# Performance work log

Measured on AMD Instinct MI355X. Metric: run time of the kernel, lower is better.

## Reference

```python
import jax, jax.numpy as jnp
import numpy as np

B, P, ED, AD, DD, E, V, T = 64, 196, 2048, 512, 512, 300, 1000, 96


def setup_inputs() -> dict:
    key = jax.random.key(0)
    ks = jax.random.split(key, 24)
    s = 0.02  # small init scale for weights
    lens = jax.random.randint(ks[2], (B,), 2, T + 1).astype(jnp.int32)
    lens = lens.at[0].set(T)  # ensure max(decode_lengths) == T-1 (static)
    return {
        'encoder_out': jax.random.normal(ks[0], (B, P, ED), jnp.float32),
        'encoded_captions': jax.random.randint(ks[1], (B, T), 0, V),
        'caption_lengths': lens,
        'emb': jax.random.uniform(ks[3], (V, E), jnp.float32, -0.1, 0.1),
        'W_enc_att': jax.random.normal(ks[4], (ED, AD), jnp.float32) * s,
        'b_enc_att': jnp.zeros((AD,), jnp.float32),
        'W_dec_att': jax.random.normal(ks[5], (DD, AD), jnp.float32) * s,
        'b_dec_att': jnp.zeros((AD,), jnp.float32),
        'w_full': jax.random.normal(ks[6], (AD,), jnp.float32) * s,
        'b_full': jnp.zeros((), jnp.float32),
        'W_init_h': jax.random.normal(ks[7], (ED, DD), jnp.float32) * s,
        'b_init_h': jnp.zeros((DD,), jnp.float32),
        'W_init_c': jax.random.normal(ks[8], (ED, DD), jnp.float32) * s,
        'b_init_c': jnp.zeros((DD,), jnp.float32),
        'W_fbeta': jax.random.normal(ks[9], (DD, ED), jnp.float32) * s,
        'b_fbeta': jnp.zeros((ED,), jnp.float32),
        'W_ih': jax.random.normal(ks[10], (E + ED, 4 * DD), jnp.float32) * s,
        'b_ih': jnp.zeros((4 * DD,), jnp.float32),
        'W_hh': jax.random.normal(ks[11], (DD, 4 * DD), jnp.float32) * s,
        'b_hh': jnp.zeros((4 * DD,), jnp.float32),
        'W_fc': jax.random.uniform(ks[12], (DD, V), jnp.float32, -0.1, 0.1),
        'b_fc': jnp.zeros((V,), jnp.float32),
    }


def reference(encoder_out, encoded_captions, caption_lengths, emb,
              W_enc_att, b_enc_att, W_dec_att, b_dec_att, w_full, b_full,
              W_init_h, b_init_h, W_init_c, b_init_c, W_fbeta, b_fbeta,
              W_ih, b_ih, W_hh, b_hh, W_fc, b_fc):
    # Sort by caption length, descending (stable like torch.sort on ints)
    sort_ind = jnp.argsort(-caption_lengths)
    lens = caption_lengths[sort_ind]
    eo = encoder_out[sort_ind]                  # [B,P,ED]
    caps = encoded_captions[sort_ind]           # [B,T]
    decode_lengths = lens - 1                   # [B]

    embs = emb[caps]                            # [B,T,E]
    mean_eo = eo.mean(axis=1)                   # [B,ED]
    h0 = mean_eo @ W_init_h + b_init_h          # [B,DD]
    c0 = mean_eo @ W_init_c + b_init_c

    # encoder-side attention projection is step-invariant: hoist it
    att1 = eo @ W_enc_att + b_enc_att           # [B,P,AD]

    Tdec = T - 1
    ts = jnp.arange(Tdec)
    masks = (decode_lengths[None, :] > ts[:, None]).astype(eo.dtype)  # [Tdec,B]
    emb_seq = jnp.swapaxes(embs[:, :Tdec, :], 0, 1)                    # [Tdec,B,E]

    def step(carry, xs):
        h, c = carry
        emb_t, m = xs                           # [B,E], [B]
        mb = m[:, None]
        # Bahdanau attention
        att2 = h @ W_dec_att + b_dec_att        # [B,AD]
        e = jnp.einsum('bpa,a->bp', jax.nn.relu(att1 + att2[:, None, :]), w_full) + b_full
        alpha = jax.nn.softmax(e, axis=1)       # [B,P]
        awe = jnp.einsum('bpd,bp->bd', eo, alpha)  # [B,ED]
        gate = jax.nn.sigmoid(h @ W_fbeta + b_fbeta)
        x = jnp.concatenate([emb_t, gate * awe], axis=1)  # [B,E+ED]
        # LSTMCell (torch gate order: i, f, g, o)
        gates = x @ W_ih + b_ih + h @ W_hh + b_hh
        i, f, g, o = jnp.split(gates, 4, axis=1)
        c_new = jax.nn.sigmoid(f) * c + jax.nn.sigmoid(i) * jnp.tanh(g)
        h_new = jax.nn.sigmoid(o) * jnp.tanh(c_new)
        # only active rows (sorted so they are a prefix) update state
        h2 = mb * h_new + (1.0 - mb) * h
        c2 = mb * c_new + (1.0 - mb) * c
        preds = (h2 @ W_fc + b_fc) * mb         # dropout = identity (eval)
        return (h2, c2), (preds, alpha * mb)

    (_, _), (preds, alphas) = jax.lax.scan(step, (h0, c0), (emb_seq, masks))
    predictions = jnp.swapaxes(preds, 0, 1)     # [B,Tdec,V]
    alphas = jnp.swapaxes(alphas, 0, 1)         # [B,Tdec,P]
    return predictions, caps, decode_lengths, alphas, sort_ind
```

## Files before the change

kernel.cpp:

```cpp
#include <hip/hip_runtime.h>
#include <stddef.h>
#include <math.h>

static constexpr int B = 64, P = 196, ED = 2048, AD = 512, DD = 512, E = 300, V = 1000, T = 96, TD = 95;
static constexpr int KX = E + ED;
static constexpr int KTOT = KX + DD;
static constexpr int KSPLIT = 8;
static constexpr int KPER = 368;
static constexpr int NG = 4 * DD;
static constexpr int NC = 2560;

static constexpr size_t POFF   = 0;
static constexpr size_t CAPOFF = (size_t)B * TD * V;
static constexpr size_t DLOFF  = CAPOFF + (size_t)B * T;
static constexpr size_t AOFF   = DLOFF + B;
static constexpr size_t SOFF   = AOFF + (size_t)B * TD * P;

__device__ __forceinline__ float sigm(float x) { return 1.0f / (1.0f + expf(-x)); }

__global__ __launch_bounds__(64) void k_sort(const int* __restrict__ lens,
                                             const int* __restrict__ caps_in,
                                             int* __restrict__ sidx,
                                             int* __restrict__ dlen,
                                             int* __restrict__ caps_s,
                                             unsigned int* __restrict__ cnt,
                                             float* __restrict__ out) {
    __shared__ int sl[B];
    __shared__ int ss[B];
    int i = threadIdx.x;
    sl[i] = lens[i];
    cnt[i] = 0u;
    cnt[i + 64] = 0u;
    __syncthreads();
    int li = sl[i];
    int r = 0;
    for (int j = 0; j < B; j++) {
        int lj = sl[j];
        r += (lj > li) || (lj == li && j < i);
    }
    ss[r] = i;
    sidx[r] = i;
    dlen[r] = li - 1;
    out[DLOFF + r] = (float)(li - 1);
    out[SOFF + r] = (float)i;
    __syncthreads();
    for (int idx = i; idx < B * T; idx += B) {
        int b = idx / T, tt = idx % T;
        int v = caps_in[ss[b] * T + tt];
        caps_s[idx] = v;
        out[CAPOFF + idx] = (float)v;
    }
}

__global__ __launch_bounds__(256) void k_emball(const float* __restrict__ emb,
                                                const int* __restrict__ caps_s,
                                                float* __restrict__ embT) {
    int t = blockIdx.x;
    int k0 = blockIdx.y * 60;
    for (int l = threadIdx.x; l < 60 * 64; l += 256) {
        int r = l >> 6, b = l & 63;
        int k = k0 + r;
        int cap = caps_s[b * T + t];
        embT[((size_t)t * E + k) * B + b] = emb[(size_t)cap * E + k];
    }
}

__global__ __launch_bounds__(256) void k_mean(const float* __restrict__ eo,
                                              const int* __restrict__ sidx,
                                              float* __restrict__ mean_eo) {
    int b = blockIdx.y;
    int d = blockIdx.x * 256 + threadIdx.x;
    const float* base = eo + ((size_t)sidx[b] * P) * ED + d;
    float s = 0.f;
    for (int p = 0; p < P; p++) s += base[(size_t)p * ED];
    mean_eo[(size_t)b * ED + d] = s * (1.0f / (float)P);
}

__global__ __launch_bounds__(256) void k_init(const float* __restrict__ mean_eo,
                                              const float* __restrict__ Wh, const float* __restrict__ bh,
                                              const float* __restrict__ Wc, const float* __restrict__ bc,
                                              float* __restrict__ h0, float* __restrict__ c0,
                                              float* __restrict__ xT) {
    int idx = blockIdx.x * 256 + threadIdx.x;
    int b = idx >> 9, j = idx & 511;
    const float* m = mean_eo + (size_t)b * ED;
    float ah = bh[j], ac = bc[j];
    for (int k = 0; k < ED; k++) {
        float mv = m[k];
        ah += mv * Wh[(size_t)k * DD + j];
        ac += mv * Wc[(size_t)k * DD + j];
    }
    h0[idx] = ah;
    c0[idx] = ac;
    xT[(size_t)(KX + DD + j) * B + b] = ah;
}

__global__ __launch_bounds__(256) void k_att1(const float* __restrict__ eo,
                                              const float* __restrict__ W,
                                              const float* __restrict__ bias,
                                              const int* __restrict__ sidx,
                                              float* __restrict__ att1) {
    int m0 = blockIdx.x * 64, n0 = blockIdx.y * 64;
    __shared__ float sA[16][68];
    __shared__ float sB[16][68];
    int tid = threadIdx.x;
    int tx = tid & 15, ty = tid >> 4;
    float acc[4][4] = {};

    int la_m = tid >> 2;
    int la_k = (tid & 3) * 4;
    int lb_k = tid >> 4;
    int lb_n = (tid & 15) * 4;

    int mA = m0 + la_m;
    int bA = mA / P, pA = mA % P;
    const float* arow = eo + ((size_t)sidx[bA] * P + pA) * ED;

    for (int k0 = 0; k0 < ED; k0 += 16) {
        float4 av = *(const float4*)(arow + k0 + la_k);
        sA[la_k + 0][la_m] = av.x;
        sA[la_k + 1][la_m] = av.y;
        sA[la_k + 2][la_m] = av.z;
        sA[la_k + 3][la_m] = av.w;
        float4 bv = *(const float4*)(W + (size_t)(k0 + lb_k) * AD + n0 + lb_n);
        *(float4*)&sB[lb_k][lb_n] = bv;
        __syncthreads();
#pragma unroll
        for (int kk = 0; kk < 16; kk++) {
            float4 a4 = *(const float4*)&sA[kk][ty * 4];
            float4 b4 = *(const float4*)&sB[kk][tx * 4];
            float av_[4] = {a4.x, a4.y, a4.z, a4.w};
            float bv_[4] = {b4.x, b4.y, b4.z, b4.w};
#pragma unroll
            for (int i = 0; i < 4; i++)
#pragma unroll
                for (int j = 0; j < 4; j++) acc[i][j] += av_[i] * bv_[j];
        }
        __syncthreads();
    }
#pragma unroll
    for (int i = 0; i < 4; i++) {
        int m = m0 + ty * 4 + i;
        int n = n0 + tx * 4;
        float4 o;
        o.x = acc[i][0] + bias[n + 0];
        o.y = acc[i][1] + bias[n + 1];
        o.z = acc[i][2] + bias[n + 2];
        o.w = acc[i][3] + bias[n + 3];
        *(float4*)(att1 + (size_t)m * AD + n) = o;
    }
}

__global__ __launch_bounds__(256) void kA1(const float* __restrict__ hprev,
                                           const float* __restrict__ Wda,
                                           const float* __restrict__ Wfb,
                                           const float* __restrict__ bda,
                                           const float* __restrict__ bfb,
                                           float* __restrict__ part1,
                                           unsigned int* __restrict__ cnt1,
                                           float* __restrict__ att2g,
                                           float* __restrict__ fg) {
    int bx = blockIdx.x;
    int nb = bx >> 2, ks = bx & 3;
    int n0 = nb * 32;
    bool is_att = (n0 < AD);
    const float* W = is_att ? Wda : Wfb;
    int ld = is_att ? AD : ED;
    int colb = is_att ? n0 : n0 - AD;
    int kbase = ks * 128;
    int tid = threadIdx.x;
    __shared__ float sH[2][16][68];
    __shared__ float sW[2][16][36];
    __shared__ unsigned int sOld;
    float acc[4][2] = {};
    int tb = tid & 15, tn = tid >> 4;
    int hb = tid >> 2, hq = tid & 3;
    int wk = tid >> 3, wn = (tid & 7) * 4;

    float4 hreg = *(const float4*)(hprev + (size_t)hb * DD + kbase + hq * 4);
    float4 wreg = make_float4(0.f, 0.f, 0.f, 0.f);
    if (tid < 128) wreg = *(const float4*)(W + (size_t)(kbase + wk) * ld + colb + wn);
    sH[0][hq * 4 + 0][hb] = hreg.x;
    sH[0][hq * 4 + 1][hb] = hreg.y;
    sH[0][hq * 4 + 2][hb] = hreg.z;
    sH[0][hq * 4 + 3][hb] = hreg.w;
    if (tid < 128) *(float4*)&sW[0][wk][wn] = wreg;
    __syncthreads();

    for (int tl = 0; tl < 8; tl++) {
        int cur = tl & 1, nxt = cur ^ 1;
        if (tl < 7) {
            int k0 = kbase + (tl + 1) * 16;
            hreg = *(const float4*)(hprev + (size_t)hb * DD + k0 + hq * 4);
            if (tid < 128) wreg = *(const float4*)(W + (size_t)(k0 + wk) * ld + colb + wn);
        }
#pragma unroll
        for (int kk = 0; kk < 16; kk++) {
            float4 hv = *(const float4*)&sH[cur][kk][tb * 4];
            float w0 = sW[cur][kk][tn * 2 + 0];
            float w1 = sW[cur][kk][tn * 2 + 1];
            acc[0][0] += hv.x * w0; acc[0][1] += hv.x * w1;
            acc[1][0] += hv.y * w0; acc[1][1] += hv.y * w1;
            acc[2][0] += hv.z * w0; acc[2][1] += hv.z * w1;
            acc[3][0] += hv.w * w0; acc[3][1] += hv.w * w1;
        }
        if (tl < 7) {
            sH[nxt][hq * 4 + 0][hb] = hreg.x;
            sH[nxt][hq * 4 + 1][hb] = hreg.y;
            sH[nxt][hq * 4 + 2][hb] = hreg.z;
            sH[nxt][hq * 4 + 3][hb] = hreg.w;
            if (tid < 128) *(float4*)&sW[nxt][wk][wn] = wreg;
        }
        __syncthreads();
    }

#pragma unroll
    for (int i = 0; i < 4; i++)
#pragma unroll
        for (int j = 0; j < 2; j++) {
            int b = tb * 4 + i, n = n0 + tn * 2 + j;
            __hip_atomic_store(&part1[((size_t)ks * B + b) * NC + n], acc[i][j],
                               __ATOMIC_RELAXED, __HIP_MEMORY_SCOPE_AGENT);
        }
    __syncthreads();
    if (tid == 0)
        sOld = __hip_atomic_fetch_add(&cnt1[nb], 1u, __ATOMIC_ACQ_REL, __HIP_MEMORY_SCOPE_AGENT);
    __syncthreads();
    if (sOld != 3u) return;

    if (tid == 0)
        __hip_atomic_store(&cnt1[nb], 0u, __ATOMIC_RELAXED, __HIP_MEMORY_SCOPE_AGENT);
#pragma unroll
    for (int rep = 0; rep < 8; rep++) {
        int idx = rep * 256 + tid;
        int b = idx >> 5, nn = idx & 31;
        int n = n0 + nn;
        float s = 0.f;
#pragma unroll
        for (int k = 0; k < 4; k++)
            s += __hip_atomic_load(&part1[((size_t)k * B + b) * NC + n],
                                   __ATOMIC_RELAXED, __HIP_MEMORY_SCOPE_AGENT);
        if (is_att) att2g[(size_t)b * AD + n] = s + bda[n];
        else {
            int d = n - AD;
            fg[(size_t)b * ED + d] = sigm(s + bfb[d]);
        }
    }
}

__global__ __launch_bounds__(256) void kA2e(const float* __restrict__ att2g,
                                            const float* __restrict__ att1,
                                            const float* __restrict__ wf,
                                            const float* __restrict__ bfv,
                                            float* __restrict__ eW) {
    int bid = blockIdx.x;
    int b = bid >> 2, ch = bid & 3;
    int tid = threadIdx.x;
    __shared__ float sa2[AD];
    __shared__ float swf[AD];
    sa2[tid] = att2g[(size_t)b * AD + tid];
    sa2[tid + 256] = att2g[(size_t)b * AD + tid + 256];
    swf[tid] = wf[tid];
    swf[tid + 256] = wf[tid + 256];
    __syncthreads();

    int w = tid >> 6, lane = tid & 63;
    float bf0 = bfv[0];
    for (int pl = w; pl < 49; pl += 4) {
        int p = ch * 49 + pl;
        const float* row = att1 + ((size_t)b * P + p) * AD + lane * 8;
        float4 u0 = *(const float4*)row;
        float4 u1 = *(const float4*)(row + 4);
        float4 s0 = *(const float4*)&sa2[lane * 8];
        float4 s1 = *(const float4*)&sa2[lane * 8 + 4];
        float4 w0 = *(const float4*)&swf[lane * 8];
        float4 w1 = *(const float4*)&swf[lane * 8 + 4];
        float acc = fmaxf(u0.x + s0.x, 0.f) * w0.x + fmaxf(u0.y + s0.y, 0.f) * w0.y +
                    fmaxf(u0.z + s0.z, 0.f) * w0.z + fmaxf(u0.w + s0.w, 0.f) * w0.w +
                    fmaxf(u1.x + s1.x, 0.f) * w1.x + fmaxf(u1.y + s1.y, 0.f) * w1.y +
                    fmaxf(u1.z + s1.z, 0.f) * w1.z + fmaxf(u1.w + s1.w, 0.f) * w1.w;
#pragma unroll
        for (int mm = 32; mm >= 1; mm >>= 1) acc += __shfl_xor(acc, mm, 64);
        if (lane == 0) eW[(size_t)b * P + p] = acc + bf0;
    }
}

__global__ __launch_bounds__(256) void kB(const float* __restrict__ eo,
                                          const int* __restrict__ sidx,
                                          const float* __restrict__ eW,
                                          const float* __restrict__ fg,
                                          const int* __restrict__ dlen,
                                          float* __restrict__ xT,
                                          float* __restrict__ out, int t) {
    int b = blockIdx.y, ch = blockIdx.x, tid = threadIdx.x;
    __shared__ float se[256];
    __shared__ float red[256];
    __shared__ float sal[P];
    __shared__ float part[4][260];

    se[tid] = (tid < P) ? eW[(size_t)b * P + tid] : -1e30f;
    __syncthreads();
    red[tid] = se[tid];
    __syncthreads();
    for (int s = 128; s > 0; s >>= 1) {
        if (tid < s) red[tid] = fmaxf(red[tid], red[tid + s]);
        __syncthreads();
    }
    float mx = red[0];
    __syncthreads();
    float ex = (tid < P) ? expf(se[tid] - mx) : 0.f;
    red[tid] = ex;
    __syncthreads();
    for (int s = 128; s > 0; s >>= 1) {
        if (tid < s) red[tid] += red[tid + s];
        __syncthreads();
    }
    float inv = 1.0f / red[0];
    if (tid < P) {
        float a = ex * inv;
        sal[tid] = a;
        if (ch == 0) {
            float m = (dlen[b] > t) ? 1.f : 0.f;
            out[AOFF + ((size_t)b * TD + t) * P + tid] = a * m;
        }
    }
    __syncthreads();

    int pg = tid >> 6, lane = tid & 63;
    int d = ch * 256 + lane * 4;
    const float* base = eo + ((size_t)sidx[b] * P) * ED + d;
    float ax = 0.f, ay = 0.f, az = 0.f, aw = 0.f;
#pragma unroll 7
    for (int i = 0; i < 49; i++) {
        int p = pg + i * 4;
        float4 v = *(const float4*)(base + (size_t)p * ED);
        float a = sal[p];
        ax += v.x * a; ay += v.y * a; az += v.z * a; aw += v.w * a;
    }
    part[pg][lane * 4 + 0] = ax;
    part[pg][lane * 4 + 1] = ay;
    part[pg][lane * 4 + 2] = az;
    part[pg][lane * 4 + 3] = aw;
    __syncthreads();
    if (tid < 64) {
        int d0 = ch * 256 + tid * 4;
        float4 g = *(const float4*)(fg + (size_t)b * ED + d0);
        float s0 = part[0][tid * 4 + 0] + part[1][tid * 4 + 0] + part[2][tid * 4 + 0] + part[3][tid * 4 + 0];
        float s1 = part[0][tid * 4 + 1] + part[1][tid * 4 + 1] + part[2][tid * 4 + 1] + part[3][tid * 4 + 1];
        float s2 = part[0][tid * 4 + 2] + part[1][tid * 4 + 2] + part[2][tid * 4 + 2] + part[3][tid * 4 + 2];
        float s3 = part[0][tid * 4 + 3] + part[1][tid * 4 + 3] + part[2][tid * 4 + 3] + part[3][tid * 4 + 3];
        xT[(size_t)(E + d0 + 0) * B + b] = g.x * s0;
        xT[(size_t)(E + d0 + 1) * B + b] = g.y * s1;
        xT[(size_t)(E + d0 + 2) * B + b] = g.z * s2;
        xT[(size_t)(E + d0 + 3) * B + b] = g.w * s3;
    }
}

__global__ __launch_bounds__(256) void kCD(const float* __restrict__ xT,
                                           const float* __restrict__ embT_t,
                                           const float* __restrict__ xh_r,
                                           const float* __restrict__ Wih,
                                           const float* __restrict__ Whh,
                                           float* __restrict__ part,
                                           unsigned int* __restrict__ cntCD,
                                           const float* __restrict__ bih,
                                           const float* __restrict__ bhh,
                                           const float* __restrict__ h0,
                                           float* __restrict__ hseq,
                                           const float* __restrict__ cread,
                                           float* __restrict__ cwrite,
                                           const int* __restrict__ dlen,
                                           float* __restrict__ xh_w, int t) {
    int bx = blockIdx.x;
    int ks = bx >> 6, nb = bx & 63;
    int n0 = nb * 32;
    int tid = threadIdx.x;
    int tb = tid & 15, tn = tid >> 4;
    int wk = tid >> 3, wn = (tid & 7) * 4;
    __shared__ float sW[2][16][36];
    __shared__ unsigned int sOld;
    float acc[4][2] = {};
    int kbase = ks * KPER;

    auto ldw = [&](int tile) -> float4 {
        int kg = kbase + tile * 16 + wk;
        float4 wv = make_float4(0.f, 0.f, 0.f, 0.f);
        if (kg < KX) wv = *(const float4*)&Wih[(size_t)kg * NG + n0 + wn];
        else if (kg < KTOT) wv = *(const float4*)&Whh[(size_t)(kg - KX) * NG + n0 + wn];
        return wv;
    };

    float4 wreg = make_float4(0.f, 0.f, 0.f, 0.f);
    if (tid < 128) {
        wreg = ldw(0);
        *(float4*)&sW[0][wk][wn] = wreg;
    }
    __syncthreads();

    for (int tile = 0; tile < 23; tile++) {
        int cur = tile & 1, nxt = cur ^ 1;
        if (tile < 22 && tid < 128) wreg = ldw(tile + 1);
#pragma unroll
        for (int kk = 0; kk < 16; kk++) {
            int kg = kbase + tile * 16 + kk;
            float4 xv = make_float4(0.f, 0.f, 0.f, 0.f);
            if (kg < E) xv = *(const float4*)&embT_t[(size_t)kg * B + tb * 4];
            else if (kg < KX) xv = *(const float4*)&xT[(size_t)kg * B + tb * 4];
            else if (kg < KTOT) xv = *(const float4*)&xh_r[(size_t)(kg - KX) * B + tb * 4];
            float w0 = sW[cur][kk][tn * 2 + 0];
            float w1 = sW[cur][kk][tn * 2 + 1];
            acc[0][0] += xv.x * w0; acc[0][1] += xv.x * w1;
            acc[1][0] += xv.y * w0; acc[1][1] += xv.y * w1;
            acc[2][0] += xv.z * w0; acc[2][1] += xv.z * w1;
            acc[3][0] += xv.w * w0; acc[3][1] += xv.w * w1;
        }
        if (tile < 22 && tid < 128) *(float4*)&sW[nxt][wk][wn] = wreg;
        __syncthreads();
    }

#pragma unroll
    for (int i = 0; i < 4; i++)
#pragma unroll
        for (int j = 0; j < 2; j++) {
            int b = tb * 4 + i, lc = tn * 2 + j;
            __hip_atomic_store(&part[((size_t)ks * B + b) * NG + n0 + lc], acc[i][j],
                               __ATOMIC_RELAXED, __HIP_MEMORY_SCOPE_AGENT);
        }
    __syncthreads();
    int jg = nb & 15;
    if (tid == 0)
        sOld = __hip_atomic_fetch_add(&cntCD[jg], 1u, __ATOMIC_ACQ_REL, __HIP_MEMORY_SCOPE_AGENT);
    __syncthreads();
    if (sOld != 31u) return;

    if (tid == 0)
        __hip_atomic_store(&cntCD[jg], 0u, __ATOMIC_RELAXED, __HIP_MEMORY_SCOPE_AGENT);

    const float* holds = (t == 0) ? h0 : (hseq + (size_t)(t - 1) * B * DD);
#pragma unroll
    for (int rep = 0; rep < 8; rep++) {
        int idx = rep * 256 + tid;
        int bb = idx >> 5;
        int jj = idx & 31;
        int j = jg * 32 + jj;
        float g4[4];
#pragma unroll
        for (int g = 0; g < 4; g++) {
            float gv = bih[g * DD + j] + bhh[g * DD + j];
#pragma unroll
            for (int s = 0; s < KSPLIT; s++)
                gv += __hip_atomic_load(&part[((size_t)s * B + bb) * NG + g * 512 + j],
                                        __ATOMIC_RELAXED, __HIP_MEMORY_SCOPE_AGENT);
            g4[g] = gv;
        }
        float cold = cread[(size_t)bb * DD + j];
        float hold = holds[(size_t)bb * DD + j];
        float cnew = sigm(g4[1]) * cold + sigm(g4[0]) * tanhf(g4[2]);
        float hnew = sigm(g4[3]) * tanhf(cnew);
        bool m = dlen[bb] > t;
        float h2 = m ? hnew : hold;
        float c2 = m ? cnew : cold;
        hseq[(size_t)t * B * DD + (size_t)bb * DD + j] = h2;
        cwrite[(size_t)bb * DD + j] = c2;
        xh_w[(size_t)j * B + bb] = h2;
    }
}

__global__ __launch_bounds__(256) void k_predsall(const float* __restrict__ hseq,
                                                  const float* __restrict__ Wfc,
                                                  const float* __restrict__ bfc,
                                                  const int* __restrict__ dlen,
                                                  float* __restrict__ out) {
    int t = blockIdx.x;
    int n0 = blockIdx.y * 64;
    int tid = threadIdx.x;
    int tx = tid & 15, ty = tid >> 4;
    __shared__ float sA[16][68];
    __shared__ float sB[16][68];
    float acc[4][4] = {};
    const float* A = hseq + (size_t)t * B * DD;

    for (int k0 = 0; k0 < DD; k0 += 16) {
        {
            int b = tid >> 2, q = tid & 3;
            float4 hv = *(const float4*)(A + (size_t)b * DD + k0 + q * 4);
            sA[q * 4 + 0][b] = hv.x;
            sA[q * 4 + 1][b] = hv.y;
            sA[q * 4 + 2][b] = hv.z;
            sA[q * 4 + 3][b] = hv.w;
        }
        {
            int kk = tid >> 4, nn = (tid & 15) * 4;
            int c = n0 + nn;
            const float* wrow = Wfc + (size_t)(k0 + kk) * V;
            float4 wv;
            if (c + 3 < V) wv = *(const float4*)(wrow + c);
            else {
                wv.x = (c + 0 < V) ? wrow[c + 0] : 0.f;
                wv.y = (c + 1 < V) ? wrow[c + 1] : 0.f;
                wv.z = (c + 2 < V) ? wrow[c + 2] : 0.f;
                wv.w = (c + 3 < V) ? wrow[c + 3] : 0.f;
            }
            *(float4*)&sB[kk][nn] = wv;
        }
        __syncthreads();
#pragma unroll
        for (int kk = 0; kk < 16; kk++) {
            float4 a4 = *(const float4*)&sA[kk][ty * 4];
            float4 b4 = *(const float4*)&sB[kk][tx * 4];
            float av_[4] = {a4.x, a4.y, a4.z, a4.w};
            float bv_[4] = {b4.x, b4.y, b4.z, b4.w};
#pragma unroll
            for (int i = 0; i < 4; i++)
#pragma unroll
                for (int j = 0; j < 4; j++) acc[i][j] += av_[i] * bv_[j];
        }
        __syncthreads();
    }
#pragma unroll
    for (int i = 0; i < 4; i++) {
        int b = ty * 4 + i;
        bool m = dlen[b] > t;
#pragma unroll
        for (int j = 0; j < 4; j++) {
            int n = n0 + tx * 4 + j;
            if (n < V)
                out[POFF + ((size_t)b * TD + t) * V + n] = m ? (acc[i][j] + bfc[n]) : 0.f;
        }
    }
}

extern "C" void kernel_launch(void* const* d_in, const int* in_sizes, int n_in,
                              void* d_out, int out_size, void* d_ws, size_t ws_size,
                              hipStream_t stream) {
    const float* eo    = (const float*)d_in[0];
    const int*   caps  = (const int*)d_in[1];
    const int*   lens  = (const int*)d_in[2];
    const float* emb   = (const float*)d_in[3];
    const float* Wea   = (const float*)d_in[4];
    const float* bea   = (const float*)d_in[5];
    const float* Wda   = (const float*)d_in[6];
    const float* bda   = (const float*)d_in[7];
    const float* wfull = (const float*)d_in[8];
    const float* bfull = (const float*)d_in[9];
    const float* Wih_  = (const float*)d_in[10];
    const float* bih_  = (const float*)d_in[11];
    const float* Wic   = (const float*)d_in[12];
    const float* bic   = (const float*)d_in[13];
    const float* Wfb   = (const float*)d_in[14];
    const float* bfb   = (const float*)d_in[15];
    const float* Wih   = (const float*)d_in[16];
    const float* bih   = (const float*)d_in[17];
    const float* Whh   = (const float*)d_in[18];
    const float* bhh   = (const float*)d_in[19];
    const float* Wfc   = (const float*)d_in[20];
    const float* bfc   = (const float*)d_in[21];
    float* out = (float*)d_out;

    char* w = (char*)d_ws;
    auto carve = [&](size_t bytes) -> void* {
        void* p = (void*)w;
        w += (bytes + 255) & ~(size_t)255;
        return p;
    };
    int* sidx      = (int*)carve(B * 4);
    int* dlen      = (int*)carve(B * 4);
    int* caps_s    = (int*)carve((size_t)B * T * 4);
    unsigned int* cnt = (unsigned int*)carve(128 * 4);
    float* mean_eo = (float*)carve((size_t)B * ED * 4);
    float* h0      = (float*)carve((size_t)B * DD * 4);
    float* cb0     = (float*)carve((size_t)B * DD * 4);
    float* cb1     = (float*)carve((size_t)B * DD * 4);
    float* att1    = (float*)carve((size_t)B * P * AD * 4);
    float* eWb     = (float*)carve((size_t)B * P * 4);
    float* att2g   = (float*)carve((size_t)B * AD * 4);
    float* fg      = (float*)carve((size_t)B * ED * 4);
    float* xT      = (float*)carve((size_t)(KTOT + DD) * B * 4);
    float* part    = (float*)carve((size_t)KSPLIT * B * NG * 4);
    float* part1   = (float*)carve((size_t)4 * B * NC * 4);
    float* hseq    = (float*)carve((size_t)TD * B * DD * 4);
    float* embT    = (float*)carve((size_t)TD * E * B * 4);
    float* cb[2] = {cb0, cb1};
    unsigned int* cnt1  = cnt;
    unsigned int* cntCD = cnt + 96;

    k_sort<<<1, 64, 0, stream>>>(lens, caps, sidx, dlen, caps_s, cnt, out);
    k_emball<<<dim3(TD, 5), 256, 0, stream>>>(emb, caps_s, embT);
    k_mean<<<dim3(ED / 256, B), 256, 0, stream>>>(eo, sidx, mean_eo);
    k_init<<<(B * DD) / 256, 256, 0, stream>>>(mean_eo, Wih_, bih_, Wic, bic, h0, cb1, xT);
    k_att1<<<dim3((B * P) / 64, AD / 64), 256, 0, stream>>>(eo, Wea, bea, sidx, att1);

    for (int t = 0; t < TD; t++) {
        const float* hprev = (t == 0) ? h0 : (hseq + (size_t)(t - 1) * B * DD);
        kA1<<<320, 256, 0, stream>>>(hprev, Wda, Wfb, bda, bfb, part1, cnt1, att2g, fg);
        kA2e<<<256, 256, 0, stream>>>(att2g, att1, wfull, bfull, eWb);
        kB<<<dim3(8, B), 256, 0, stream>>>(eo, sidx, eWb, fg, dlen, xT, out, t);
        const float* xh_r = xT + (size_t)(KX + ((t + 1) & 1) * DD) * B;
        float*       xh_w = xT + (size_t)(KX + (t & 1) * DD) * B;
        kCD<<<512, 256, 0, stream>>>(xT, embT + (size_t)t * E * B, xh_r, Wih, Whh, part, cntCD,
                                     bih, bhh, h0, hseq, cb[(t + 1) & 1], cb[t & 1], dlen, xh_w, t);
    }
    k_predsall<<<dim3(TD, 16), 256, 0, stream>>>(hseq, Wfc, bfc, dlen, out);
}
```

Measured before the change: 16.87 ms.

## Fuse per-timestep kernels into one persistent cooperative kernel with grid syncs

Replaces the four kernel launches per decode step (95 steps, 380 launches) with one cooperative persistent kernel of 512 blocks. Each step runs the four phases separated by grid.sync(), and shared memory is reused through a union. The goal is to remove per-launch overhead and kernel-boundary drains in the sequential recurrence. In exchange, it depends on all 512 blocks being co-resident at launch_bounds(256,2) and adds grid-wide barrier cost. Phases with fewer active blocks leave the other blocks idle.

```diff
diff --git a/kernel.cpp b/kernel.cpp
--- a/kernel.cpp
+++ b/kernel.cpp
@@ -1,6 +1,9 @@
 #include <hip/hip_runtime.h>
+#include <hip/hip_cooperative_groups.h>
 #include <stddef.h>
 #include <math.h>
+
+namespace cg = cooperative_groups;
 
 static constexpr int B = 64, P = 196, ED = 2048, AD = 512, DD = 512, E = 300, V = 1000, T = 96, TD = 95;
 static constexpr int KX = E + ED;
@@ -151,318 +154,312 @@
     }
 }
 
-__global__ __launch_bounds__(256) void kA1(const float* __restrict__ hprev,
-                                           const float* __restrict__ Wda,
-                                           const float* __restrict__ Wfb,
-                                           const float* __restrict__ bda,
-                                           const float* __restrict__ bfb,
-                                           float* __restrict__ part1,
-                                           unsigned int* __restrict__ cnt1,
-                                           float* __restrict__ att2g,
-                                           float* __restrict__ fg) {
-    int bx = blockIdx.x;
-    int nb = bx >> 2, ks = bx & 3;
-    int n0 = nb * 32;
-    bool is_att = (n0 < AD);
-    const float* W = is_att ? Wda : Wfb;
-    int ld = is_att ? AD : ED;
-    int colb = is_att ? n0 : n0 - AD;
-    int kbase = ks * 128;
-    int tid = threadIdx.x;
-    __shared__ float sH[2][16][68];
-    __shared__ float sW[2][16][36];
-    __shared__ unsigned int sOld;
-    float acc[4][2] = {};
-    int tb = tid & 15, tn = tid >> 4;
-    int hb = tid >> 2, hq = tid & 3;
-    int wk = tid >> 3, wn = (tid & 7) * 4;
-
-    float4 hreg = *(const float4*)(hprev + (size_t)hb * DD + kbase + hq * 4);
-    float4 wreg = make_float4(0.f, 0.f, 0.f, 0.f);
-    if (tid < 128) wreg = *(const float4*)(W + (size_t)(kbase + wk) * ld + colb + wn);
-    sH[0][hq * 4 + 0][hb] = hreg.x;
-    sH[0][hq * 4 + 1][hb] = hreg.y;
-    sH[0][hq * 4 + 2][hb] = hreg.z;
-    sH[0][hq * 4 + 3][hb] = hreg.w;
-    if (tid < 128) *(float4*)&sW[0][wk][wn] = wreg;
-    __syncthreads();
-
-    for (int tl = 0; tl < 8; tl++) {
-        int cur = tl & 1, nxt = cur ^ 1;
-        if (tl < 7) {
-            int k0 = kbase + (tl + 1) * 16;
-            hreg = *(const float4*)(hprev + (size_t)hb * DD + k0 + hq * 4);
-            if (tid < 128) wreg = *(const float4*)(W + (size_t)(k0 + wk) * ld + colb + wn);
-        }
-#pragma unroll
-        for (int kk = 0; kk < 16; kk++) {
-            float4 hv = *(const float4*)&sH[cur][kk][tb * 4];
-            float w0 = sW[cur][kk][tn * 2 + 0];
-            float w1 = sW[cur][kk][tn * 2 + 1];
-            acc[0][0] += hv.x * w0; acc[0][1] += hv.x * w1;
-            acc[1][0] += hv.y * w0; acc[1][1] += hv.y * w1;
-            acc[2][0] += hv.z * w0; acc[2][1] += hv.z * w1;
-            acc[3][0] += hv.w * w0; acc[3][1] += hv.w * w1;
-        }
-        if (tl < 7) {
-            sH[nxt][hq * 4 + 0][hb] = hreg.x;
-            sH[nxt][hq * 4 + 1][hb] = hreg.y;
-            sH[nxt][hq * 4 + 2][hb] = hreg.z;
-            sH[nxt][hq * 4 + 3][hb] = hreg.w;
-            if (tid < 128) *(float4*)&sW[nxt][wk][wn] = wreg;
-        }
-        __syncthreads();
-    }
-
-#pragma unroll
-    for (int i = 0; i < 4; i++)
-#pragma unroll
-        for (int j = 0; j < 2; j++) {
-            int b = tb * 4 + i, n = n0 + tn * 2 + j;
-            __hip_atomic_store(&part1[((size_t)ks * B + b) * NC + n], acc[i][j],
-                               __ATOMIC_RELAXED, __HIP_MEMORY_SCOPE_AGENT);
-        }
-    __syncthreads();
-    if (tid == 0)
-        sOld = __hip_atomic_fetch_add(&cnt1[nb], 1u, __ATOMIC_ACQ_REL, __HIP_MEMORY_SCOPE_AGENT);
-    __syncthreads();
-    if (sOld != 3u) return;
-
-    if (tid == 0)
-        __hip_atomic_store(&cnt1[nb], 0u, __ATOMIC_RELAXED, __HIP_MEMORY_SCOPE_AGENT);
-#pragma unroll
-    for (int rep = 0; rep < 8; rep++) {
-        int idx = rep * 256 + tid;
-        int b = idx >> 5, nn = idx & 31;
-        int n = n0 + nn;
-        float s = 0.f;
-#pragma unroll
-        for (int k = 0; k < 4; k++)
-            s += __hip_atomic_load(&part1[((size_t)k * B + b) * NC + n],
-                                   __ATOMIC_RELAXED, __HIP_MEMORY_SCOPE_AGENT);
-        if (is_att) att2g[(size_t)b * AD + n] = s + bda[n];
-        else {
-            int d = n - AD;
-            fg[(size_t)b * ED + d] = sigm(s + bfb[d]);
-        }
-    }
-}
-
-__global__ __launch_bounds__(256) void kA2e(const float* __restrict__ att2g,
-                                            const float* __restrict__ att1,
-                                            const float* __restrict__ wf,
-                                            const float* __restrict__ bfv,
-                                            float* __restrict__ eW) {
-    int bid = blockIdx.x;
-    int b = bid >> 2, ch = bid & 3;
-    int tid = threadIdx.x;
-    __shared__ float sa2[AD];
-    __shared__ float swf[AD];
-    sa2[tid] = att2g[(size_t)b * AD + tid];
-    sa2[tid + 256] = att2g[(size_t)b * AD + tid + 256];
-    swf[tid] = wf[tid];
-    swf[tid + 256] = wf[tid + 256];
-    __syncthreads();
-
-    int w = tid >> 6, lane = tid & 63;
-    float bf0 = bfv[0];
-    for (int pl = w; pl < 49; pl += 4) {
-        int p = ch * 49 + pl;
-        const float* row = att1 + ((size_t)b * P + p) * AD + lane * 8;
-        float4 u0 = *(const float4*)row;
-        float4 u1 = *(const float4*)(row + 4);
-        float4 s0 = *(const float4*)&sa2[lane * 8];
-        float4 s1 = *(const float4*)&sa2[lane * 8 + 4];
-        float4 w0 = *(const float4*)&swf[lane * 8];
-        float4 w1 = *(const float4*)&swf[lane * 8 + 4];
-        float acc = fmaxf(u0.x + s0.x, 0.f) * w0.x + fmaxf(u0.y + s0.y, 0.f) * w0.y +
-                    fmaxf(u0.z + s0.z, 0.f) * w0.z + fmaxf(u0.w + s0.w, 0.f) * w0.w +
-                    fmaxf(u1.x + s1.x, 0.f) * w1.x + fmaxf(u1.y + s1.y, 0.f) * w1.y +
-                    fmaxf(u1.z + s1.z, 0.f) * w1.z + fmaxf(u1.w + s1.w, 0.f) * w1.w;
-#pragma unroll
-        for (int mm = 32; mm >= 1; mm >>= 1) acc += __shfl_xor(acc, mm, 64);
-        if (lane == 0) eW[(size_t)b * P + p] = acc + bf0;
-    }
-}
-
-__global__ __launch_bounds__(256) void kB(const float* __restrict__ eo,
-                                          const int* __restrict__ sidx,
-                                          const float* __restrict__ eW,
-                                          const float* __restrict__ fg,
-                                          const int* __restrict__ dlen,
-                                          float* __restrict__ xT,
-                                          float* __restrict__ out, int t) {
-    int b = blockIdx.y, ch = blockIdx.x, tid = threadIdx.x;
-    __shared__ float se[256];
-    __shared__ float red[256];
-    __shared__ float sal[P];
-    __shared__ float part[4][260];
-
-    se[tid] = (tid < P) ? eW[(size_t)b * P + tid] : -1e30f;
-    __syncthreads();
-    red[tid] = se[tid];
-    __syncthreads();
-    for (int s = 128; s > 0; s >>= 1) {
-        if (tid < s) red[tid] = fmaxf(red[tid], red[tid + s]);
-        __syncthreads();
-    }
-    float mx = red[0];
-    __syncthreads();
-    float ex = (tid < P) ? expf(se[tid] - mx) : 0.f;
-    red[tid] = ex;
-    __syncthreads();
-    for (int s = 128; s > 0; s >>= 1) {
-        if (tid < s) red[tid] += red[tid + s];
-        __syncthreads();
-    }
-    float inv = 1.0f / red[0];
-    if (tid < P) {
-        float a = ex * inv;
-        sal[tid] = a;
-        if (ch == 0) {
-            float m = (dlen[b] > t) ? 1.f : 0.f;
-            out[AOFF + ((size_t)b * TD + t) * P + tid] = a * m;
-        }
-    }
-    __syncthreads();
-
-    int pg = tid >> 6, lane = tid & 63;
-    int d = ch * 256 + lane * 4;
-    const float* base = eo + ((size_t)sidx[b] * P) * ED + d;
-    float ax = 0.f, ay = 0.f, az = 0.f, aw = 0.f;
+union SM {
+    struct { float sH[2][16][68]; float sW[2][16][36]; unsigned int sOld; } p1;
+    struct { float sa2[AD]; float swf[AD]; } p2;
+    struct { float se[256]; float red[256]; float sal[200]; float part[4][260]; } p3;
+    struct { float sW[2][16][36]; unsigned int sOld; } p4;
+};
+
+__global__ __launch_bounds__(256, 2) void k_steps2(
+    const float* __restrict__ eo, const int* __restrict__ sidx,
+    const int* __restrict__ dlen,
+    const float* __restrict__ Wda, const float* __restrict__ Wfb,
+    const float* __restrict__ bda, const float* __restrict__ bfb,
+    const float* __restrict__ wfull, const float* __restrict__ bfull,
+    const float* __restrict__ att1,
+    const float* __restrict__ Wih, const float* __restrict__ Whh,
+    const float* __restrict__ bih, const float* __restrict__ bhh,
+    const float* __restrict__ h0, float* __restrict__ cb0, float* __restrict__ cb1,
+    float* __restrict__ part1, unsigned int* __restrict__ cnt1,
+    float* __restrict__ att2g, float* __restrict__ fg,
+    float* __restrict__ eW, float* __restrict__ xT,
+    float* __restrict__ gpart, unsigned int* __restrict__ cntCD,
+    const float* __restrict__ embT, float* __restrict__ hseq,
+    float* __restrict__ out)
+{
+    cg::grid_group grid = cg::this_grid();
+    const int bid = blockIdx.x;
+    const int tid = threadIdx.x;
+    __shared__ SM sm;
+
+#pragma unroll 1
+    for (int t = 0; t < TD; t++) {
+        const float* hprev = (t == 0) ? h0 : (hseq + (size_t)(t - 1) * B * DD);
+
+        if (bid < 320) {
+            int nb = bid >> 2, ks = bid & 3;
+            int n0 = nb * 32;
+            bool is_att = (n0 < AD);
+            const float* W = is_att ? Wda : Wfb;
+            int ld = is_att ? AD : ED;
+            int colb = is_att ? n0 : n0 - AD;
+            int kbase = ks * 128;
+            float acc[4][2] = {};
+            int tb = tid & 15, tn = tid >> 4;
+            int hb = tid >> 2, hq = tid & 3;
+            int wk = tid >> 3, wn = (tid & 7) * 4;
+
+            float4 hreg = *(const float4*)(hprev + (size_t)hb * DD + kbase + hq * 4);
+            float4 wreg = make_float4(0.f, 0.f, 0.f, 0.f);
+            if (tid < 128) wreg = *(const float4*)(W + (size_t)(kbase + wk) * ld + colb + wn);
+            sm.p1.sH[0][hq * 4 + 0][hb] = hreg.x;
+            sm.p1.sH[0][hq * 4 + 1][hb] = hreg.y;
+            sm.p1.sH[0][hq * 4 + 2][hb] = hreg.z;
+            sm.p1.sH[0][hq * 4 + 3][hb] = hreg.w;
+            if (tid < 128) *(float4*)&sm.p1.sW[0][wk][wn] = wreg;
+            __syncthreads();
+
+            for (int tl = 0; tl < 8; tl++) {
+                int cur = tl & 1, nxt = cur ^ 1;
+                if (tl < 7) {
+                    int k0 = kbase + (tl + 1) * 16;
+                    hreg = *(const float4*)(hprev + (size_t)hb * DD + k0 + hq * 4);
+                    if (tid < 128) wreg = *(const float4*)(W + (size_t)(k0 + wk) * ld + colb + wn);
+                }
+#pragma unroll
+                for (int kk = 0; kk < 16; kk++) {
+                    float4 hv = *(const float4*)&sm.p1.sH[cur][kk][tb * 4];
+                    float w0 = sm.p1.sW[cur][kk][tn * 2 + 0];
+                    float w1 = sm.p1.sW[cur][kk][tn * 2 + 1];
+                    acc[0][0] += hv.x * w0; acc[0][1] += hv.x * w1;
+                    acc[1][0] += hv.y * w0; acc[1][1] += hv.y * w1;
+                    acc[2][0] += hv.z * w0; acc[2][1] += hv.z * w1;
+                    acc[3][0] += hv.w * w0; acc[3][1] += hv.w * w1;
+                }
+                if (tl < 7) {
+                    sm.p1.sH[nxt][hq * 4 + 0][hb] = hreg.x;
+                    sm.p1.sH[nxt][hq * 4 + 1][hb] = hreg.y;
+                    sm.p1.sH[nxt][hq * 4 + 2][hb] = hreg.z;
+                    sm.p1.sH[nxt][hq * 4 + 3][hb] = hreg.w;
+                    if (tid < 128) *(float4*)&sm.p1.sW[nxt][wk][wn] = wreg;
+                }
+                __syncthreads();
+            }
+
+#pragma unroll
+            for (int i = 0; i < 4; i++)
+#pragma unroll
+                for (int j = 0; j < 2; j++) {
+                    int b = tb * 4 + i, n = n0 + tn * 2 + j;
+                    __hip_atomic_store(&part1[((size_t)ks * B + b) * NC + n], acc[i][j],
+                                       __ATOMIC_RELAXED, __HIP_MEMORY_SCOPE_AGENT);
+                }
+            __syncthreads();
+            if (tid == 0)
+                sm.p1.sOld = __hip_atomic_fetch_add(&cnt1[nb], 1u, __ATOMIC_ACQ_REL, __HIP_MEMORY_SCOPE_AGENT);
+            __syncthreads();
+            if (sm.p1.sOld == 3u) {
+                if (tid == 0)
+                    __hip_atomic_store(&cnt1[nb], 0u, __ATOMIC_RELAXED, __HIP_MEMORY_SCOPE_AGENT);
+#pragma unroll
+                for (int rep = 0; rep < 8; rep++) {
+                    int idx = rep * 256 + tid;
+                    int b = idx >> 5, nn = idx & 31;
+                    int n = n0 + nn;
+                    float s = 0.f;
+#pragma unroll
+                    for (int k = 0; k < 4; k++)
+                        s += __hip_atomic_load(&part1[((size_t)k * B + b) * NC + n],
+                                               __ATOMIC_RELAXED, __HIP_MEMORY_SCOPE_AGENT);
+                    if (is_att) att2g[(size_t)b * AD + n] = s + bda[n];
+                    else {
+                        int d = n - AD;
+                        fg[(size_t)b * ED + d] = sigm(s + bfb[d]);
+                    }
+                }
+            }
+        }
+        grid.sync();
+
+        if (bid < 256) {
+            int b = bid >> 2, ch = bid & 3;
+            sm.p2.sa2[tid] = att2g[(size_t)b * AD + tid];
+            sm.p2.sa2[tid + 256] = att2g[(size_t)b * AD + tid + 256];
+            sm.p2.swf[tid] = wfull[tid];
+            sm.p2.swf[tid + 256] = wfull[tid + 256];
+            __syncthreads();
+
+            int w = tid >> 6, lane = tid & 63;
+            float bf0 = bfull[0];
+            for (int pl = w; pl < 49; pl += 4) {
+                int p = ch * 49 + pl;
+                const float* row = att1 + ((size_t)b * P + p) * AD + lane * 8;
+                float4 u0 = *(const float4*)row;
+                float4 u1 = *(const float4*)(row + 4);
+                float4 s0 = *(const float4*)&sm.p2.sa2[lane * 8];
+                float4 s1 = *(const float4*)&sm.p2.sa2[lane * 8 + 4];
+                float4 w0 = *(const float4*)&sm.p2.swf[lane * 8];
+                float4 w1 = *(const float4*)&sm.p2.swf[lane * 8 + 4];
+                float acc = fmaxf(u0.x + s0.x, 0.f) * w0.x + fmaxf(u0.y + s0.y, 0.f) * w0.y +
+                            fmaxf(u0.z + s0.z, 0.f) * w0.z + fmaxf(u0.w + s0.w, 0.f) * w0.w +
+                            fmaxf(u1.x + s1.x, 0.f) * w1.x + fmaxf(u1.y + s1.y, 0.f) * w1.y +
+                            fmaxf(u1.z + s1.z, 0.f) * w1.z + fmaxf(u1.w + s1.w, 0.f) * w1.w;
+#pragma unroll
+                for (int mm = 32; mm >= 1; mm >>= 1) acc += __shfl_xor(acc, mm, 64);
+                if (lane == 0) eW[(size_t)b * P + p] = acc + bf0;
+            }
+        }
+        grid.sync();
+
+        {
+            int b = bid >> 3, ch = bid & 7;
+            sm.p3.se[tid] = (tid < P) ? eW[(size_t)b * P + tid] : -1e30f;
+            __syncthreads();
+            sm.p3.red[tid] = sm.p3.se[tid];
+            __syncthreads();
+            for (int s = 128; s > 0; s >>= 1) {
+                if (tid < s) sm.p3.red[tid] = fmaxf(sm.p3.red[tid], sm.p3.red[tid + s]);
+                __syncthreads();
+            }
+            float mx = sm.p3.red[0];
+            __syncthreads();
+            float ex = (tid < P) ? expf(sm.p3.se[tid] - mx) : 0.f;
+            sm.p3.red[tid] = ex;
+            __syncthreads();
+            for (int s = 128; s > 0; s >>= 1) {
+                if (tid < s) sm.p3.red[tid] += sm.p3.red[tid + s];
+                __syncthreads();
+            }
+            float inv = 1.0f / sm.p3.red[0];
+            if (tid < P) {
+                float a = ex * inv;
+                sm.p3.sal[tid] = a;
+                if (ch == 0) {
+                    float m = (dlen[b] > t) ? 1.f : 0.f;
+                    out[AOFF + ((size_t)b * TD + t) * P + tid] = a * m;
+                }
+            }
+            __syncthreads();
+
+            int pg = tid >> 6, lane = tid & 63;
+            int d = ch * 256 + lane * 4;
+            const float* base = eo + ((size_t)sidx[b] * P) * ED + d;
+            float ax = 0.f, ay = 0.f, az = 0.f, aw = 0.f;
 #pragma unroll 7
-    for (int i = 0; i < 49; i++) {
-        int p = pg + i * 4;
-        float4 v = *(const float4*)(base + (size_t)p * ED);
-        float a = sal[p];
-        ax += v.x * a; ay += v.y * a; az += v.z * a; aw += v.w * a;
-    }
-    part[pg][lane * 4 + 0] = ax;
-    part[pg][lane * 4 + 1] = ay;
-    part[pg][lane * 4 + 2] = az;
-    part[pg][lane * 4 + 3] = aw;
-    __syncthreads();
-    if (tid < 64) {
-        int d0 = ch * 256 + tid * 4;
-        float4 g = *(const float4*)(fg + (size_t)b * ED + d0);
-        float s0 = part[0][tid * 4 + 0] + part[1][tid * 4 + 0] + part[2][tid * 4 + 0] + part[3][tid * 4 + 0];
-        float s1 = part[0][tid * 4 + 1] + part[1][tid * 4 + 1] + part[2][tid * 4 + 1] + part[3][tid * 4 + 1];
-        float s2 = part[0][tid * 4 + 2] + part[1][tid * 4 + 2] + part[2][tid * 4 + 2] + part[3][tid * 4 + 2];
-        float s3 = part[0][tid * 4 + 3] + part[1][tid * 4 + 3] + part[2][tid * 4 + 3] + part[3][tid * 4 + 3];
-        xT[(size_t)(E + d0 + 0) * B + b] = g.x * s0;
-        xT[(size_t)(E + d0 + 1) * B + b] = g.y * s1;
-        xT[(size_t)(E + d0 + 2) * B + b] = g.z * s2;
-        xT[(size_t)(E + d0 + 3) * B + b] = g.w * s3;
-    }
-}
-
-__global__ __launch_bounds__(256) void kCD(const float* __restrict__ xT,
-                                           const float* __restrict__ embT_t,
-                                           const float* __restrict__ xh_r,
-                                           const float* __restrict__ Wih,
-                                           const float* __restrict__ Whh,
-                                           float* __restrict__ part,
-                                           unsigned int* __restrict__ cntCD,
-                                           const float* __restrict__ bih,
-                                           const float* __restrict__ bhh,
-                                           const float* __restrict__ h0,
-                                           float* __restrict__ hseq,
-                                           const float* __restrict__ cread,
-                                           float* __restrict__ cwrite,
-                                           const int* __restrict__ dlen,
-                                           float* __restrict__ xh_w, int t) {
-    int bx = blockIdx.x;
-    int ks = bx >> 6, nb = bx & 63;
-    int n0 = nb * 32;
-    int tid = threadIdx.x;
-    int tb = tid & 15, tn = tid >> 4;
-    int wk = tid >> 3, wn = (tid & 7) * 4;
-    __shared__ float sW[2][16][36];
-    __shared__ unsigned int sOld;
-    float acc[4][2] = {};
-    int kbase = ks * KPER;
-
-    auto ldw = [&](int tile) -> float4 {
-        int kg = kbase + tile * 16 + wk;
-        float4 wv = make_float4(0.f, 0.f, 0.f, 0.f);
-        if (kg < KX) wv = *(const float4*)&Wih[(size_t)kg * NG + n0 + wn];
-        else if (kg < KTOT) wv = *(const float4*)&Whh[(size_t)(kg - KX) * NG + n0 + wn];
-        return wv;
-    };
-
-    float4 wreg = make_float4(0.f, 0.f, 0.f, 0.f);
-    if (tid < 128) {
-        wreg = ldw(0);
-        *(float4*)&sW[0][wk][wn] = wreg;
-    }
-    __syncthreads();
-
-    for (int tile = 0; tile < 23; tile++) {
-        int cur = tile & 1, nxt = cur ^ 1;
-        if (tile < 22 && tid < 128) wreg = ldw(tile + 1);
-#pragma unroll
-        for (int kk = 0; kk < 16; kk++) {
-            int kg = kbase + tile * 16 + kk;
-            float4 xv = make_float4(0.f, 0.f, 0.f, 0.f);
-            if (kg < E) xv = *(const float4*)&embT_t[(size_t)kg * B + tb * 4];
-            else if (kg < KX) xv = *(const float4*)&xT[(size_t)kg * B + tb * 4];
-            else if (kg < KTOT) xv = *(const float4*)&xh_r[(size_t)(kg - KX) * B + tb * 4];
-            float w0 = sW[cur][kk][tn * 2 + 0];
-            float w1 = sW[cur][kk][tn * 2 + 1];
-            acc[0][0] += xv.x * w0; acc[0][1] += xv.x * w1;
-            acc[1][0] += xv.y * w0; acc[1][1] += xv.y * w1;
-            acc[2][0] += xv.z * w0; acc[2][1] += xv.z * w1;
-            acc[3][0] += xv.w * w0; acc[3][1] += xv.w * w1;
-        }
-        if (tile < 22 && tid < 128) *(float4*)&sW[nxt][wk][wn] = wreg;
-        __syncthreads();
-    }
-
-#pragma unroll
-    for (int i = 0; i < 4; i++)
-#pragma unroll
-        for (int j = 0; j < 2; j++) {
-            int b = tb * 4 + i, lc = tn * 2 + j;
-            __hip_atomic_store(&part[((size_t)ks * B + b) * NG + n0 + lc], acc[i][j],
-                               __ATOMIC_RELAXED, __HIP_MEMORY_SCOPE_AGENT);
-        }
-    __syncthreads();
-    int jg = nb & 15;
-    if (tid == 0)
-        sOld = __hip_atomic_fetch_add(&cntCD[jg], 1u, __ATOMIC_ACQ_REL, __HIP_MEMORY_SCOPE_AGENT);
-    __syncthreads();
-    if (sOld != 31u) return;
-
-    if (tid == 0)
-        __hip_atomic_store(&cntCD[jg], 0u, __ATOMIC_RELAXED, __HIP_MEMORY_SCOPE_AGENT);
-
-    const float* holds = (t == 0) ? h0 : (hseq + (size_t)(t - 1) * B * DD);
-#pragma unroll
-    for (int rep = 0; rep < 8; rep++) {
-        int idx = rep * 256 + tid;
-        int bb = idx >> 5;
-        int jj = idx & 31;
-        int j = jg * 32 + jj;
-        float g4[4];
-#pragma unroll
-        for (int g = 0; g < 4; g++) {
-            float gv = bih[g * DD + j] + bhh[g * DD + j];
-#pragma unroll
-            for (int s = 0; s < KSPLIT; s++)
-                gv += __hip_atomic_load(&part[((size_t)s * B + bb) * NG + g * 512 + j],
-                                        __ATOMIC_RELAXED, __HIP_MEMORY_SCOPE_AGENT);
-            g4[g] = gv;
-        }
-        float cold = cread[(size_t)bb * DD + j];
-        float hold = holds[(size_t)bb * DD + j];
-        float cnew = sigm(g4[1]) * cold + sigm(g4[0]) * tanhf(g4[2]);
-        float hnew = sigm(g4[3]) * tanhf(cnew);
-        bool m = dlen[bb] > t;
-        float h2 = m ? hnew : hold;
-        float c2 = m ? cnew : cold;
-        hseq[(size_t)t * B * DD + (size_t)bb * DD + j] = h2;
-        cwrite[(size_t)bb * DD + j] = c2;
-        xh_w[(size_t)j * B + bb] = h2;
+            for (int i = 0; i < 49; i++) {
+                int p = pg + i * 4;
+                float4 v = *(const float4*)(base + (size_t)p * ED);
+                float a = sm.p3.sal[p];
+                ax += v.x * a; ay += v.y * a; az += v.z * a; aw += v.w * a;
+            }
+            sm.p3.part[pg][lane * 4 + 0] = ax;
+            sm.p3.part[pg][lane * 4 + 1] = ay;
+            sm.p3.part[pg][lane * 4 + 2] = az;
+            sm.p3.part[pg][lane * 4 + 3] = aw;
+            __syncthreads();
+            if (tid < 64) {
+                int d0 = ch * 256 + tid * 4;
+                float4 g = *(const float4*)(fg + (size_t)b * ED + d0);
+                float s0 = sm.p3.part[0][tid * 4 + 0] + sm.p3.part[1][tid * 4 + 0] + sm.p3.part[2][tid * 4 + 0] + sm.p3.part[3][tid * 4 + 0];
+                float s1 = sm.p3.part[0][tid * 4 + 1] + sm.p3.part[1][tid * 4 + 1] + sm.p3.part[2][tid * 4 + 1] + sm.p3.part[3][tid * 4 + 1];
+                float s2 = sm.p3.part[0][tid * 4 + 2] + sm.p3.part[1][tid * 4 + 2] + sm.p3.part[2][tid * 4 + 2] + sm.p3.part[3][tid * 4 + 2];
+                float s3 = sm.p3.part[0][tid * 4 + 3] + sm.p3.part[1][tid * 4 + 3] + sm.p3.part[2][tid * 4 + 3] + sm.p3.part[3][tid * 4 + 3];
+                xT[(size_t)(E + d0 + 0) * B + b] = g.x * s0;
+                xT[(size_t)(E + d0 + 1) * B + b] = g.y * s1;
+                xT[(size_t)(E + d0 + 2) * B + b] = g.z * s2;
+                xT[(size_t)(E + d0 + 3) * B + b] = g.w * s3;
+            }
+        }
+        grid.sync();
+
+        {
+            const float* embT_t = embT + (size_t)t * E * B;
+            const float* xh_r = xT + (size_t)(KX + ((t + 1) & 1) * DD) * B;
+            float*       xh_w = xT + (size_t)(KX + (t & 1) * DD) * B;
+            const float* cread  = ((t + 1) & 1) ? cb1 : cb0;
+            float*       cwrite = (t & 1) ? cb1 : cb0;
+
+            int ks = bid >> 6, nb = bid & 63;
+            int n0 = nb * 32;
+            int tb = tid & 15, tn = tid >> 4;
+            int wk = tid >> 3, wn = (tid & 7) * 4;
+            float acc[4][2] = {};
+            int kbase = ks * KPER;
+
+            auto ldw = [&](int tile) -> float4 {
+                int kg = kbase + tile * 16 + wk;
+                float4 wv = make_float4(0.f, 0.f, 0.f, 0.f);
+                if (kg < KX) wv = *(const float4*)&Wih[(size_t)kg * NG + n0 + wn];
+                else if (kg < KTOT) wv = *(const float4*)&Whh[(size_t)(kg - KX) * NG + n0 + wn];
+                return wv;
+            };
+
+            float4 wreg = make_float4(0.f, 0.f, 0.f, 0.f);
+            if (tid < 128) {
+                wreg = ldw(0);
+                *(float4*)&sm.p4.sW[0][wk][wn] = wreg;
+            }
+            __syncthreads();
+
+            for (int tile = 0; tile < 23; tile++) {
+                int cur = tile & 1, nxt = cur ^ 1;
+                if (tile < 22 && tid < 128) wreg = ldw(tile + 1);
+#pragma unroll
+                for (int kk = 0; kk < 16; kk++) {
+                    int kg = kbase + tile * 16 + kk;
+                    float4 xv = make_float4(0.f, 0.f, 0.f, 0.f);
+                    if (kg < E) xv = *(const float4*)&embT_t[(size_t)kg * B + tb * 4];
+                    else if (kg < KX) xv = *(const float4*)&xT[(size_t)kg * B + tb * 4];
+                    else if (kg < KTOT) xv = *(const float4*)&xh_r[(size_t)(kg - KX) * B + tb * 4];
+                    float w0 = sm.p4.sW[cur][kk][tn * 2 + 0];
+                    float w1 = sm.p4.sW[cur][kk][tn * 2 + 1];
+                    acc[0][0] += xv.x * w0; acc[0][1] += xv.x * w1;
+                    acc[1][0] += xv.y * w0; acc[1][1] += xv.y * w1;
+                    acc[2][0] += xv.z * w0; acc[2][1] += xv.z * w1;
+                    acc[3][0] += xv.w * w0; acc[3][1] += xv.w * w1;
+                }
+                if (tile < 22 && tid < 128) *(float4*)&sm.p4.sW[nxt][wk][wn] = wreg;
+                __syncthreads();
+            }
+
+#pragma unroll
+            for (int i = 0; i < 4; i++)
+#pragma unroll
+                for (int j = 0; j < 2; j++) {
+                    int b = tb * 4 + i, lc = tn * 2 + j;
+                    __hip_atomic_store(&gpart[((size_t)ks * B + b) * NG + n0 + lc], acc[i][j],
+                                       __ATOMIC_RELAXED, __HIP_MEMORY_SCOPE_AGENT);
+                }
+            __syncthreads();
+            int jg = nb & 15;
+            if (tid == 0)
+                sm.p4.sOld = __hip_atomic_fetch_add(&cntCD[jg], 1u, __ATOMIC_ACQ_REL, __HIP_MEMORY_SCOPE_AGENT);
+            __syncthreads();
+            if (sm.p4.sOld == 31u) {
+                if (tid == 0)
+                    __hip_atomic_store(&cntCD[jg], 0u, __ATOMIC_RELAXED, __HIP_MEMORY_SCOPE_AGENT);
+                const float* holds = (t == 0) ? h0 : (hseq + (size_t)(t - 1) * B * DD);
+#pragma unroll
+                for (int rep = 0; rep < 8; rep++) {
+                    int idx = rep * 256 + tid;
+                    int bb = idx >> 5;
+                    int jj = idx & 31;
+                    int j = jg * 32 + jj;
+                    float g4[4];
+#pragma unroll
+                    for (int g = 0; g < 4; g++) {
+                        float gv = bih[g * DD + j] + bhh[g * DD + j];
+#pragma unroll
+                        for (int s = 0; s < KSPLIT; s++)
+                            gv += __hip_atomic_load(&gpart[((size_t)s * B + bb) * NG + g * 512 + j],
+                                                    __ATOMIC_RELAXED, __HIP_MEMORY_SCOPE_AGENT);
+                        g4[g] = gv;
+                    }
+                    float cold = cread[(size_t)bb * DD + j];
+                    float hold = holds[(size_t)bb * DD + j];
+                    float cnew = sigm(g4[1]) * cold + sigm(g4[0]) * tanhf(g4[2]);
+                    float hnew = sigm(g4[3]) * tanhf(cnew);
+                    bool m = dlen[bb] > t;
+                    float h2 = m ? hnew : hold;
+                    float c2 = m ? cnew : cold;
+                    hseq[(size_t)t * B * DD + (size_t)bb * DD + j] = h2;
+                    cwrite[(size_t)bb * DD + j] = c2;
+                    xh_w[(size_t)j * B + bb] = h2;
+                }
+            }
+        }
+        grid.sync();
     }
 }
 
@@ -576,11 +573,10 @@
     float* att2g   = (float*)carve((size_t)B * AD * 4);
     float* fg      = (float*)carve((size_t)B * ED * 4);
     float* xT      = (float*)carve((size_t)(KTOT + DD) * B * 4);
-    float* part    = (float*)carve((size_t)KSPLIT * B * NG * 4);
+    float* gpart   = (float*)carve((size_t)KSPLIT * B * NG * 4);
     float* part1   = (float*)carve((size_t)4 * B * NC * 4);
     float* hseq    = (float*)carve((size_t)TD * B * DD * 4);
     float* embT    = (float*)carve((size_t)TD * E * B * 4);
-    float* cb[2] = {cb0, cb1};
     unsigned int* cnt1  = cnt;
     unsigned int* cntCD = cnt + 96;
 
@@ -590,15 +586,17 @@
     k_init<<<(B * DD) / 256, 256, 0, stream>>>(mean_eo, Wih_, bih_, Wic, bic, h0, cb1, xT);
     k_att1<<<dim3((B * P) / 64, AD / 64), 256, 0, stream>>>(eo, Wea, bea, sidx, att1);
 
-    for (int t = 0; t < TD; t++) {
-        const float* hprev = (t == 0) ? h0 : (hseq + (size_t)(t - 1) * B * DD);
-        kA1<<<320, 256, 0, stream>>>(hprev, Wda, Wfb, bda, bfb, part1, cnt1, att2g, fg);
-        kA2e<<<256, 256, 0, stream>>>(att2g, att1, wfull, bfull, eWb);
-        kB<<<dim3(8, B), 256, 0, stream>>>(eo, sidx, eWb, fg, dlen, xT, out, t);
-        const float* xh_r = xT + (size_t)(KX + ((t + 1) & 1) * DD) * B;
-        float*       xh_w = xT + (size_t)(KX + (t & 1) * DD) * B;
-        kCD<<<512, 256, 0, stream>>>(xT, embT + (size_t)t * E * B, xh_r, Wih, Whh, part, cntCD,
-                                     bih, bhh, h0, hseq, cb[(t + 1) & 1], cb[t & 1], dlen, xh_w, t);
-    }
+    void* kargs[] = {
+        (void*)&eo, (void*)&sidx, (void*)&dlen,
+        (void*)&Wda, (void*)&Wfb, (void*)&bda, (void*)&bfb,
+        (void*)&wfull, (void*)&bfull, (void*)&att1,
+        (void*)&Wih, (void*)&Whh, (void*)&bih, (void*)&bhh,
+        (void*)&h0, (void*)&cb0, (void*)&cb1,
+        (void*)&part1, (void*)&cnt1, (void*)&att2g, (void*)&fg,
+        (void*)&eWb, (void*)&xT, (void*)&gpart, (void*)&cntCD,
+        (void*)&embT, (void*)&hseq, (void*)&out
+    };
+    hipLaunchCooperativeKernel((void*)k_steps2, dim3(512), dim3(256), kargs, 0, stream);
+
     k_predsall<<<dim3(TD, 16), 256, 0, stream>>>(hseq, Wfc, bfc, dlen, out);
 }
```

New measurement: 53.14 ms. 3.15x slower.
